# Kernel tuning notes

Hardware: AMD Instinct MI355X
Metric: run time of the kernel (lower is better)

Reference implementation:

```python
import jax, jax.numpy as jnp
import numpy as np

IN = 128; HID = 128; OUT = 128; HEADS = 3; T1 = 0.2; T2 = 0.2
B = 512; L = 32; V = 100000; NMETA = 5


def _corr_full(s, t):
    # s, t: (B, L, E, N). Full cross-correlation along last axis.
    # Matches F.conv1d(hs, ht, groups=BLE, padding=N-1): out[k] = sum_m s[k+m-(N-1)] * t[m]
    N = s.shape[-1]
    sp = jnp.pad(s, ((0, 0), (0, 0), (0, 0), (N - 1, N - 1)))
    out = jnp.stack([(sp[..., k:k + N] * t).sum(-1) for k in range(2 * N - 1)], axis=-1)
    return jnp.swapaxes(out, -1, -2)  # (B, L, 2N-1, E)


def _node_att(h, Wt, Ws, Wc):
    # h: (B, L, P, E); Wt/Ws/Wc: (HEADS, E, HID)
    Bh, Lh, P, E = h.shape
    H = h.reshape(Bh * Lh, P, E)
    hi = jnp.einsum('ne,heo->hno', H[:, 0], Wt)                 # target-node projection
    logits = jnp.einsum('npe,heo,hno->hnp', H, Ws, hi) / T1     # (heads, BL, P)
    alpha = jax.nn.softmax(logits, axis=-1)                     # softmax over path positions
    Z = jnp.einsum('hnp,npe,heo->no', alpha, H, Wc) / HEADS     # mean over heads
    return Z.reshape(Bh, Lh, -1)


def _forward(emb_user, emb_item, emb_attr1, emb_attr2, emb_attr3, Wt, Ws, Wc,
             pw1, pb1, pw2, fw1, fb1, fw2, fb2,
             UI, IU, UIUI, IUIU, UIAI1, IAIU1, UIAI2, IAIU2, UIAI3, IAIU3):
    src = emb_user[UI[:, 0, 0]]
    tgt = emb_item[IU[:, 0, 0]]
    ui = jnp.stack([emb_user[UI[..., 0]], emb_item[UI[..., 1]]], axis=3)
    iu = jnp.stack([emb_item[IU[..., 0]], emb_user[IU[..., 1]]], axis=3)

    def p4(tabs, idx):
        return jnp.stack([tabs[k][idx[..., k]] for k in range(4)], axis=3)

    uiui = p4([emb_user, emb_item, emb_user, emb_item], UIUI)
    iuiu = p4([emb_item, emb_user, emb_item, emb_user], IUIU)
    uiai1 = p4([emb_user, emb_item, emb_attr1, emb_item], UIAI1)
    iaiu1 = p4([emb_item, emb_attr1, emb_item, emb_user], IAIU1)
    uiai2 = p4([emb_user, emb_item, emb_attr2, emb_item], UIAI2)
    iaiu2 = p4([emb_item, emb_attr2, emb_item, emb_user], IAIU2)
    uiai3 = p4([emb_user, emb_item, emb_attr3, emb_item], UIAI3)
    iaiu3 = p4([emb_item, emb_attr3, emb_item, emb_user], IAIU3)

    user_feats = [ui, uiui, uiai1, uiai2, uiai3]
    item_feats = [iu, iuiu, iaiu1, iaiu2, iaiu3]
    Hs = [_node_att(_corr_full(uf, itf), Wt[m], Ws[m], Wc[m])
          for m, (uf, itf) in enumerate(zip(user_feats, item_feats))]
    Z = jnp.stack(Hs, 1)                        # (B, 5, L, HID)
    z = Z.reshape(Z.shape[0], -1, HID)          # (B, 5L, HID)
    w = jnp.tanh(z @ pw1 + pb1) @ pw2 / T2      # (B, 5L, 1)
    beta = jax.nn.softmax(w, axis=1)
    path_out = (beta * z).sum(1)                # (B, HID)
    x = jnp.concatenate([src, tgt, path_out], axis=1)
    x = jax.nn.relu(x @ fw1 + fb1)              # dropout in eval mode -> identity
    return jax.nn.sigmoid(x @ fw2 + fb2)        # (B, 1)


def setup_inputs() -> dict:
    key = jax.random.key(0)
    ks = jax.random.split(key, 24)

    def idx(k, n):
        return jax.random.randint(k, (B, L, n), 0, V, dtype=jnp.int32)

    d = {
        'UI': idx(ks[0], 2), 'IU': idx(ks[1], 2),
        'UIUI': idx(ks[2], 4), 'IUIU': idx(ks[3], 4),
        'UIAI1': idx(ks[4], 4), 'IAIU1': idx(ks[5], 4),
        'UIAI2': idx(ks[6], 4), 'IAIU2': idx(ks[7], 4),
        'UIAI3': idx(ks[8], 4), 'IAIU3': idx(ks[9], 4),
    }

    def emb(k):
        t = jax.random.normal(k, (V + 1, IN), jnp.float32) * 0.05
        return t.at[0].set(0.0)  # padding_idx=0

    d['emb_user'] = emb(ks[10]); d['emb_item'] = emb(ks[11])
    d['emb_attr1'] = emb(ks[12]); d['emb_attr2'] = emb(ks[13]); d['emb_attr3'] = emb(ks[14])
    s = (2.0 / (IN + HID)) ** 0.5  # xavier scale
    d['Wt'] = jax.random.normal(ks[15], (NMETA, HEADS, IN, HID), jnp.float32) * s
    d['Ws'] = jax.random.normal(ks[16], (NMETA, HEADS, IN, HID), jnp.float32) * s
    d['Wc'] = jax.random.normal(ks[17], (NMETA, HEADS, IN, HID), jnp.float32) * s
    d['pw1'] = jax.random.normal(ks[18], (HID, HID), jnp.float32) * s
    d['pb1'] = jnp.zeros((HID,), jnp.float32)
    d['pw2'] = jax.random.normal(ks[19], (HID, 1), jnp.float32) * s
    d['fw1'] = jax.random.normal(ks[20], (3 * HID, OUT), jnp.float32) * 0.02
    d['fb1'] = jnp.zeros((OUT,), jnp.float32)
    d['fw2'] = jax.random.normal(ks[21], (OUT, 1), jnp.float32) * 0.02
    d['fb2'] = jnp.zeros((1,), jnp.float32)
    return d


def reference(UI, IU, UIUI, IUIU, UIAI1, IAIU1, UIAI2, IAIU2, UIAI3, IAIU3,
              emb_user, emb_item, emb_attr1, emb_attr2, emb_attr3,
              Wt, Ws, Wc, pw1, pb1, pw2, fw1, fb1, fw2, fb2):
    return _forward(emb_user, emb_item, emb_attr1, emb_attr2, emb_attr3, Wt, Ws, Wc,
                    pw1, pb1, pw2, fw1, fb1, fw2, fb2,
                    UI, IU, UIUI, IUIU, UIAI1, IAIU1, UIAI2, IAIU2, UIAI3, IAIU3)
```

## Files before the change

### kernel.cpp

```cpp
#include <hip/hip_runtime.h>
#include <hip/hip_bf16.h>
#include <cstdint>
#include <cstddef>


typedef __hip_bfloat16 bf16;
typedef __attribute__((ext_vector_type(8))) short  bfrag;
typedef __attribute__((ext_vector_type(4))) float  ffrag;

#define NNODES 16384

__device__ __forceinline__ float bflo(uint32_t u) { return __uint_as_float(u << 16); }
__device__ __forceinline__ float bfhi(uint32_t u) { return __uint_as_float(u & 0xffff0000u); }

__global__ __launch_bounds__(256) void build_BmatT(
    const float* __restrict__ Ws, const float* __restrict__ Wt,
    bf16* __restrict__ BmT)
{
  int mh = blockIdx.x >> 4;
  int g  = blockIdx.x & 15;
  int m = mh / 3, h = mh % 3;
  const float* ws = Ws + (size_t)mh * 16384;
  const float* wt = Wt + (size_t)mh * 16384;
  int tid = threadIdx.x;
  int e = tid & 127, half = tid >> 7;
  __shared__ float wtl[2][128];
  for (int ep0 = g * 8; ep0 < g * 8 + 8; ep0 += 2) {
    int ep = ep0 + half;
    wtl[half][e] = wt[ep * 128 + e];
    __syncthreads();
    float acc = 0.f;
    #pragma unroll 4
    for (int o = 0; o < 128; ++o) acc += ws[e * 128 + o] * wtl[half][o];
    BmT[((size_t)(m * 384 + h * 128 + e)) * 128 + ep] = __float2bfloat16(acc);
    __syncthreads();
  }
}

__global__ __launch_bounds__(256) void conv_WcT(
    const float* __restrict__ Wc, bf16* __restrict__ WcT)
{
  int idx = blockIdx.x * 256 + threadIdx.x;
  int he = idx % 384, mo = idx / 384;
  int m = mo >> 7, o = mo & 127;
  WcT[idx] = __float2bfloat16(Wc[((size_t)m * 384 + he) * 128 + o]);
}

__global__ __launch_bounds__(256) void conv_pw1T(
    const float* __restrict__ pw1, bf16* __restrict__ pw1T)
{
  int idx = blockIdx.x * 256 + threadIdx.x;
  int o = idx >> 7, k = idx & 127;
  pw1T[idx] = __float2bfloat16(pw1[(size_t)k * 128 + o]);
}

template <int P>
__global__ __launch_bounds__(512) void fused_metapath(
    const float* __restrict__ Tu0, const float* __restrict__ Tu1,
    const float* __restrict__ Tu2, const float* __restrict__ Tu3,
    const float* __restrict__ Tt0, const float* __restrict__ Tt1,
    const float* __restrict__ Tt2, const float* __restrict__ Tt3,
    const int* __restrict__ idxU, const int* __restrict__ idxT,
    const bf16* __restrict__ BmT,
    const bf16* __restrict__ WcT,
    float* __restrict__ Zall, int m)
{
  constexpr int PP = 2 * P - 1;
  constexpr int NS = PP * 136;
  constexpr int NPAIR = 3 * PP;
  __shared__ bf16 Hs[16 * NS];
  __shared__ bf16 Ss[16 * 392];
  __shared__ float lg[16][3][8];
  __shared__ float alpha[16][3][8];

  int tid = threadIdx.x;
  int lane = tid & 63, wid = tid >> 6;
  int l15 = lane & 15, l4 = lane >> 4;
  int n0 = blockIdx.x * 16;

  {
    const float* TU[4] = {Tu0, Tu1, Tu2, Tu3};
    const float* TT[4] = {Tt0, Tt1, Tt2, Tt3};
    int e = tid & 127;
    #pragma unroll
    for (int g = 0; g < 4; ++g) {
      int ln = g * 4 + (tid >> 7);
      int n = n0 + ln;
      float su[P], st[P];
      #pragma unroll
      for (int p = 0; p < P; ++p) {
        su[p] = TU[p][(size_t)idxU[n * P + p] * 128 + e];
        st[p] = TT[p][(size_t)idxT[n * P + p] * 128 + e];
      }
      bf16* Hn = &Hs[ln * NS + e];
      #pragma unroll
      for (int k = 0; k < PP; ++k) {
        float acc = 0.f;
        #pragma unroll
        for (int i = 0; i < P; ++i) {
          int j = k + i - (P - 1);
          if (j >= 0 && j < P) acc += su[j] * st[i];
        }
        Hn[k * 136] = __float2bfloat16(acc);
      }
    }
  }
  __syncthreads();

  {
    bfrag a[4];
    #pragma unroll
    for (int kk = 0; kk < 4; ++kk)
      a[kk] = *(const bfrag*)&Hs[l15 * NS + kk * 32 + 8 * l4];
    #pragma unroll
    for (int f = 0; f < 3; ++f) {
      int col = wid * 48 + f * 16 + l15;
      ffrag acc = {0.f, 0.f, 0.f, 0.f};
      #pragma unroll
      for (int kk = 0; kk < 4; ++kk) {
        bfrag b = *(const bfrag*)&BmT[(size_t)col * 128 + kk * 32 + 8 * l4];
        acc = __builtin_amdgcn_mfma_f32_16x16x32_bf16(a[kk], b, acc, 0, 0, 0);
      }
      #pragma unroll
      for (int r = 0; r < 4; ++r) {
        int node = 4 * l4 + r;
        Ss[node * 392 + col] = __float2bfloat16(acc[r]);
      }
    }
  }
  __syncthreads();

  {
    int node = tid >> 5, q = tid & 31;
    if (q < NPAIR) {
      int h = q / PP, p = q - h * PP;
      const uint32_t* hrow = (const uint32_t*)&Hs[node * NS + p * 136];
      const uint32_t* srow = (const uint32_t*)&Ss[node * 392 + h * 128];
      float acc = 0.f;
      #pragma unroll 8
      for (int i = 0; i < 64; ++i) {
        uint32_t hv = hrow[i], sv = srow[i];
        acc += bflo(hv) * bflo(sv) + bfhi(hv) * bfhi(sv);
      }
      lg[node][h][p] = acc * 5.0f;
    }
  }
  __syncthreads();

  if (tid < 48) {
    int nd = tid / 3, h = tid - nd * 3;
    float mx = -1e30f;
    #pragma unroll
    for (int p = 0; p < PP; ++p) mx = fmaxf(mx, lg[nd][h][p]);
    float s = 0.f, ev[8];
    #pragma unroll
    for (int p = 0; p < PP; ++p) { ev[p] = expf(lg[nd][h][p] - mx); s += ev[p]; }
    float inv = 1.0f / s;
    #pragma unroll
    for (int p = 0; p < PP; ++p) alpha[nd][h][p] = ev[p] * inv;
  }
  __syncthreads();

  {
    int node = tid >> 5, q = tid & 31;
    #pragma unroll
    for (int c = 0; c < 6; ++c) {
      int o2 = q * 6 + c;
      int h = o2 >> 6, e = (o2 & 63) * 2;
      float a0 = 0.f, a1 = 0.f;
      #pragma unroll
      for (int p = 0; p < PP; ++p) {
        float al = alpha[node][h][p];
        uint32_t hv = *(const uint32_t*)&Hs[node * NS + p * 136 + e];
        a0 += al * bflo(hv);
        a1 += al * bfhi(hv);
      }
      Ss[node * 392 + h * 128 + e]     = __float2bfloat16(a0);
      Ss[node * 392 + h * 128 + e + 1] = __float2bfloat16(a1);
    }
  }
  __syncthreads();

  {
    bfrag a[12];
    #pragma unroll
    for (int kk = 0; kk < 12; ++kk)
      a[kk] = *(const bfrag*)&Ss[l15 * 392 + kk * 32 + 8 * l4];
    int col = wid * 16 + l15;
    ffrag acc = {0.f, 0.f, 0.f, 0.f};
    #pragma unroll
    for (int kk = 0; kk < 12; ++kk) {
      bfrag b = *(const bfrag*)&WcT[(size_t)col * 384 + kk * 32 + 8 * l4];
      acc = __builtin_amdgcn_mfma_f32_16x16x32_bf16(a[kk], b, acc, 0, 0, 0);
    }
    #pragma unroll
    for (int r = 0; r < 4; ++r) {
      int gn = n0 + 4 * l4 + r;
      int crow = (((gn >> 5) * 5 + m) << 5) + (gn & 31);
      Zall[(size_t)crow * 128 + col] = acc[r] * (1.0f / 3.0f);
    }
  }
}

__global__ __launch_bounds__(256) void fused_tail(
    const float* __restrict__ Zall,
    const bf16* __restrict__ pw1T,
    const float* __restrict__ pb1, const float* __restrict__ pw2,
    const int* __restrict__ UI, const int* __restrict__ IU,
    const float* __restrict__ emb_user, const float* __restrict__ emb_item,
    const float* __restrict__ fw1, const float* __restrict__ fb1,
    const float* __restrict__ fw2, const float* __restrict__ fb2,
    float* __restrict__ out)
{
  __shared__ bf16 Zs[160 * 136];
  __shared__ float wrow[160];
  __shared__ float ph[2][128];
  __shared__ float xs[384];
  __shared__ float mx_s, denom_s;
  __shared__ float yred[2];

  int b = blockIdx.x, tid = threadIdx.x;
  int lane = tid & 63, wid = tid >> 6;
  int l15 = lane & 15, l4 = lane >> 4;

  {
    const float4* src = (const float4*)(Zall + (size_t)b * 160 * 128);
    #pragma unroll
    for (int i = 0; i < 20; ++i) {
      int v = i * 256 + tid;
      int row = v >> 5, c4 = v & 31;
      float4 x = src[v];
      bf16* d = &Zs[row * 136 + c4 * 4];
      d[0] = __float2bfloat16(x.x); d[1] = __float2bfloat16(x.y);
      d[2] = __float2bfloat16(x.z); d[3] = __float2bfloat16(x.w);
    }
  }
  __syncthreads();

  for (int rf = wid; rf < 10; rf += 4) {
    bfrag a[4];
    #pragma unroll
    for (int kk = 0; kk < 4; ++kk)
      a[kk] = *(const bfrag*)&Zs[(rf * 16 + l15) * 136 + kk * 32 + 8 * l4];
    float part[4] = {0.f, 0.f, 0.f, 0.f};
    #pragma unroll
    for (int f = 0; f < 8; ++f) {
      int col = f * 16 + l15;
      ffrag acc = {0.f, 0.f, 0.f, 0.f};
      #pragma unroll
      for (int kk = 0; kk < 4; ++kk) {
        bfrag bv = *(const bfrag*)&pw1T[(size_t)col * 128 + kk * 32 + 8 * l4];
        acc = __builtin_amdgcn_mfma_f32_16x16x32_bf16(a[kk], bv, acc, 0, 0, 0);
      }
      float bias = pb1[col], w2 = pw2[col];
      #pragma unroll
      for (int r = 0; r < 4; ++r) part[r] += tanhf(acc[r] + bias) * w2;
    }
    #pragma unroll
    for (int d = 1; d < 16; d <<= 1) {
      #pragma unroll
      for (int r = 0; r < 4; ++r) part[r] += __shfl_xor(part[r], d);
    }
    if (l15 == 0) {
      #pragma unroll
      for (int r = 0; r < 4; ++r)
        wrow[rf * 16 + 4 * l4 + r] = part[r] * 5.0f;
    }
  }
  __syncthreads();

  if (tid == 0) {
    float mx = -1e30f;
    for (int j = 0; j < 160; ++j) mx = fmaxf(mx, wrow[j]);
    float s = 0.f;
    for (int j = 0; j < 160; ++j) s += expf(wrow[j] - mx);
    mx_s = mx; denom_s = s;
  }
  __syncthreads();
  {
    float mx = mx_s, inv = 1.0f / denom_s;
    if (tid < 160) wrow[tid] = expf(wrow[tid] - mx) * inv;
  }
  __syncthreads();

  {
    int e = tid & 127, half = tid >> 7;
    float acc = 0.f;
    #pragma unroll 4
    for (int j = half * 80; j < half * 80 + 80; ++j)
      acc += wrow[j] * __bfloat162float(Zs[j * 136 + e]);
    ph[half][e] = acc;
  }
  __syncthreads();

  {
    int su = UI[b * 64];
    int ti = IU[b * 64];
    if (tid < 128) {
      xs[tid]       = emb_user[(size_t)su * 128 + tid];
      xs[256 + tid] = ph[0][tid] + ph[1][tid];
    } else {
      xs[tid]       = emb_item[(size_t)ti * 128 + (tid - 128)];
    }
  }
  __syncthreads();

  {
    int o = tid & 127, half = tid >> 7;
    float acc = 0.f;
    #pragma unroll 4
    for (int i = half * 192; i < half * 192 + 192; ++i)
      acc += xs[i] * fw1[(size_t)i * 128 + o];
    __syncthreads();
    ph[half][o] = acc;
  }
  __syncthreads();
  if (tid < 128) {
    float y = fmaxf(ph[0][tid] + ph[1][tid] + fb1[tid], 0.0f) * fw2[tid];
    #pragma unroll
    for (int off = 32; off; off >>= 1) y += __shfl_down(y, off);
    if ((tid & 63) == 0) yred[tid >> 6] = y;
  }
  __syncthreads();
  if (tid == 0) {
    float s = yred[0] + yred[1] + fb2[0];
    out[b] = 1.0f / (1.0f + expf(-s));
  }
}

extern "C" void kernel_launch(void* const* d_in, const int* in_sizes, int n_in,
                              void* d_out, int out_size, void* d_ws, size_t ws_size,
                              hipStream_t stream)
{
  const int* UI    = (const int*)d_in[0];
  const int* IU    = (const int*)d_in[1];
  const int* UIUI  = (const int*)d_in[2];
  const int* IUIU  = (const int*)d_in[3];
  const int* UIAI1 = (const int*)d_in[4];
  const int* IAIU1 = (const int*)d_in[5];
  const int* UIAI2 = (const int*)d_in[6];
  const int* IAIU2 = (const int*)d_in[7];
  const int* UIAI3 = (const int*)d_in[8];
  const int* IAIU3 = (const int*)d_in[9];
  const float* emb_user = (const float*)d_in[10];
  const float* emb_item = (const float*)d_in[11];
  const float* emb_a1   = (const float*)d_in[12];
  const float* emb_a2   = (const float*)d_in[13];
  const float* emb_a3   = (const float*)d_in[14];
  const float* Wt  = (const float*)d_in[15];
  const float* Ws  = (const float*)d_in[16];
  const float* Wc  = (const float*)d_in[17];
  const float* pw1 = (const float*)d_in[18];
  const float* pb1 = (const float*)d_in[19];
  const float* pw2 = (const float*)d_in[20];
  const float* fw1 = (const float*)d_in[21];
  const float* fb1 = (const float*)d_in[22];
  const float* fw2 = (const float*)d_in[23];
  const float* fb2 = (const float*)d_in[24];
  float* out = (float*)d_out;

  char* wsb = (char*)d_ws;
  bf16*  BmT  = (bf16*)wsb;
  bf16*  WcT  = (bf16*)(wsb + 491520);
  bf16*  pw1T = (bf16*)(wsb + 983040);
  float* Zall = (float*)(wsb + 1015808);

  build_BmatT<<<240, 256, 0, stream>>>(Ws, Wt, BmT);
  conv_WcT<<<960, 256, 0, stream>>>(Wc, WcT);
  conv_pw1T<<<64, 256, 0, stream>>>(pw1, pw1T);

  const float* u2[5] = {nullptr, emb_user, emb_a1, emb_a2, emb_a3};
  const float* t1[5] = {emb_user, emb_user, emb_a1, emb_a2, emb_a3};
  const int* idxU[5] = {UI, UIUI, UIAI1, UIAI2, UIAI3};
  const int* idxT[5] = {IU, IUIU, IAIU1, IAIU2, IAIU3};

  for (int m = 0; m < 5; ++m) {
    if (m == 0) {
      fused_metapath<2><<<1024, 512, 0, stream>>>(
          emb_user, emb_item, nullptr, nullptr,
          emb_item, emb_user, nullptr, nullptr,
          idxU[m], idxT[m], BmT, WcT, Zall, m);
    } else {
      fused_metapath<4><<<1024, 512, 0, stream>>>(
          emb_user, emb_item, u2[m], emb_item,
          emb_item, t1[m], emb_item, emb_user,
          idxU[m], idxT[m],
          BmT + (size_t)m * 384 * 128, WcT + (size_t)m * 128 * 384, Zall, m);
    }
  }

  fused_tail<<<512, 256, 0, stream>>>(Zall, pw1T, pb1, pw2,
                                      UI, IU, emb_user, emb_item,
                                      fw1, fb1, fw2, fb2, out);
}
```

Measured before the change: 245.5 us.

## Merge metapath launches into one kernel, store Zall as bf16, widen tail

Replaces the five per-metapath launches with a single 5120-block kernel that picks the metapath from the block index and uses dynamic shared memory. It also hoists all embedding gathers ahead of the correlation compute so more loads are in flight, and stores the intermediate Z in bf16 to halve its traffic. The tail kernel moves to 512 threads, uses vectorized bf16 copies, and replaces the single-thread softmax with a wave-shuffle reduction. Costs are higher register pressure from the hoisted gathers, lower occupancy from the dynamic shared allocation, and bf16 rounding of Z before the tail.

```diff
diff --git a/kernel.cpp b/kernel.cpp
--- a/kernel.cpp
+++ b/kernel.cpp
@@ -55,7 +55,8 @@
 }
 
 template <int P>
-__global__ __launch_bounds__(512) void fused_metapath(
+__device__ __forceinline__ void metapath_body(
+    char* smem,
     const float* __restrict__ Tu0, const float* __restrict__ Tu1,
     const float* __restrict__ Tu2, const float* __restrict__ Tu3,
     const float* __restrict__ Tt0, const float* __restrict__ Tt1,
@@ -63,35 +64,38 @@
     const int* __restrict__ idxU, const int* __restrict__ idxT,
     const bf16* __restrict__ BmT,
     const bf16* __restrict__ WcT,
-    float* __restrict__ Zall, int m)
+    bf16* __restrict__ Zall, int m, int tile)
 {
   constexpr int PP = 2 * P - 1;
   constexpr int NS = PP * 136;
   constexpr int NPAIR = 3 * PP;
-  __shared__ bf16 Hs[16 * NS];
-  __shared__ bf16 Ss[16 * 392];
-  __shared__ float lg[16][3][8];
-  __shared__ float alpha[16][3][8];
+  bf16*  Hs    = (bf16*)smem;
+  bf16*  Ss    = (bf16*)(smem + 16 * NS * 2);
+  float* lg    = (float*)(smem + 16 * NS * 2 + 16 * 392 * 2);
+  float* alpha = lg + 16 * 3 * 8;
 
   int tid = threadIdx.x;
   int lane = tid & 63, wid = tid >> 6;
   int l15 = lane & 15, l4 = lane >> 4;
-  int n0 = blockIdx.x * 16;
+  int n0 = tile * 16;
 
   {
     const float* TU[4] = {Tu0, Tu1, Tu2, Tu3};
     const float* TT[4] = {Tt0, Tt1, Tt2, Tt3};
     int e = tid & 127;
+    float su[4][P], st[4][P];
+    #pragma unroll
+    for (int g = 0; g < 4; ++g) {
+      int n = n0 + g * 4 + (tid >> 7);
+      #pragma unroll
+      for (int p = 0; p < P; ++p) {
+        su[g][p] = TU[p][(size_t)idxU[n * P + p] * 128 + e];
+        st[g][p] = TT[p][(size_t)idxT[n * P + p] * 128 + e];
+      }
+    }
     #pragma unroll
     for (int g = 0; g < 4; ++g) {
       int ln = g * 4 + (tid >> 7);
-      int n = n0 + ln;
-      float su[P], st[P];
-      #pragma unroll
-      for (int p = 0; p < P; ++p) {
-        su[p] = TU[p][(size_t)idxU[n * P + p] * 128 + e];
-        st[p] = TT[p][(size_t)idxT[n * P + p] * 128 + e];
-      }
       bf16* Hn = &Hs[ln * NS + e];
       #pragma unroll
       for (int k = 0; k < PP; ++k) {
@@ -99,7 +103,7 @@
         #pragma unroll
         for (int i = 0; i < P; ++i) {
           int j = k + i - (P - 1);
-          if (j >= 0 && j < P) acc += su[j] * st[i];
+          if (j >= 0 && j < P) acc += su[g][j] * st[g][i];
         }
         Hn[k * 136] = __float2bfloat16(acc);
       }
@@ -142,22 +146,21 @@
         uint32_t hv = hrow[i], sv = srow[i];
         acc += bflo(hv) * bflo(sv) + bfhi(hv) * bfhi(sv);
       }
-      lg[node][h][p] = acc * 5.0f;
+      lg[(node * 3 + h) * 8 + p] = acc * 5.0f;
     }
   }
   __syncthreads();
 
   if (tid < 48) {
-    int nd = tid / 3, h = tid - nd * 3;
     float mx = -1e30f;
     #pragma unroll
-    for (int p = 0; p < PP; ++p) mx = fmaxf(mx, lg[nd][h][p]);
+    for (int p = 0; p < PP; ++p) mx = fmaxf(mx, lg[tid * 8 + p]);
     float s = 0.f, ev[8];
     #pragma unroll
-    for (int p = 0; p < PP; ++p) { ev[p] = expf(lg[nd][h][p] - mx); s += ev[p]; }
+    for (int p = 0; p < PP; ++p) { ev[p] = expf(lg[tid * 8 + p] - mx); s += ev[p]; }
     float inv = 1.0f / s;
     #pragma unroll
-    for (int p = 0; p < PP; ++p) alpha[nd][h][p] = ev[p] * inv;
+    for (int p = 0; p < PP; ++p) alpha[tid * 8 + p] = ev[p] * inv;
   }
   __syncthreads();
 
@@ -170,7 +173,7 @@
       float a0 = 0.f, a1 = 0.f;
       #pragma unroll
       for (int p = 0; p < PP; ++p) {
-        float al = alpha[node][h][p];
+        float al = alpha[(node * 3 + h) * 8 + p];
         uint32_t hv = *(const uint32_t*)&Hs[node * NS + p * 136 + e];
         a0 += al * bflo(hv);
         a1 += al * bfhi(hv);
@@ -197,13 +200,47 @@
     for (int r = 0; r < 4; ++r) {
       int gn = n0 + 4 * l4 + r;
       int crow = (((gn >> 5) * 5 + m) << 5) + (gn & 31);
-      Zall[(size_t)crow * 128 + col] = acc[r] * (1.0f / 3.0f);
-    }
-  }
-}
-
-__global__ __launch_bounds__(256) void fused_tail(
-    const float* __restrict__ Zall,
+      Zall[(size_t)crow * 128 + col] = __float2bfloat16(acc[r] * (1.0f / 3.0f));
+    }
+  }
+}
+
+__global__ __launch_bounds__(512) void fused_all(
+    const float* __restrict__ emb_user, const float* __restrict__ emb_item,
+    const float* __restrict__ emb_a1, const float* __restrict__ emb_a2,
+    const float* __restrict__ emb_a3,
+    const int* __restrict__ UI,    const int* __restrict__ IU,
+    const int* __restrict__ UIUI,  const int* __restrict__ IUIU,
+    const int* __restrict__ UIAI1, const int* __restrict__ IAIU1,
+    const int* __restrict__ UIAI2, const int* __restrict__ IAIU2,
+    const int* __restrict__ UIAI3, const int* __restrict__ IAIU3,
+    const bf16* __restrict__ BmT, const bf16* __restrict__ WcT,
+    bf16* __restrict__ Zall)
+{
+  extern __shared__ char smem[];
+  int bid = blockIdx.x;
+  int m = bid >> 10, tile = bid & 1023;
+  if (m == 0) {
+    metapath_body<2>(smem, emb_user, emb_item, nullptr, nullptr,
+                     emb_item, emb_user, nullptr, nullptr,
+                     UI, IU, BmT, WcT, Zall, 0, tile);
+  } else {
+    const float* u2 = (m == 1) ? emb_user : (m == 2) ? emb_a1
+                    : (m == 3) ? emb_a2 : emb_a3;
+    const int* iu_ = (m == 1) ? UIUI : (m == 2) ? UIAI1
+                   : (m == 3) ? UIAI2 : UIAI3;
+    const int* it_ = (m == 1) ? IUIU : (m == 2) ? IAIU1
+                   : (m == 3) ? IAIU2 : IAIU3;
+    metapath_body<4>(smem, emb_user, emb_item, u2, emb_item,
+                     emb_item, u2, emb_item, emb_user,
+                     iu_, it_,
+                     BmT + (size_t)m * 49152, WcT + (size_t)m * 49152,
+                     Zall, m, tile);
+  }
+}
+
+__global__ __launch_bounds__(512) void fused_tail(
+    const bf16* __restrict__ Zall,
     const bf16* __restrict__ pw1T,
     const float* __restrict__ pb1, const float* __restrict__ pw2,
     const int* __restrict__ UI, const int* __restrict__ IU,
@@ -214,9 +251,9 @@
 {
   __shared__ bf16 Zs[160 * 136];
   __shared__ float wrow[160];
-  __shared__ float ph[2][128];
+  __shared__ float ph[4][128];
   __shared__ float xs[384];
-  __shared__ float mx_s, denom_s;
+  __shared__ float sred[16];
   __shared__ float yred[2];
 
   int b = blockIdx.x, tid = threadIdx.x;
@@ -225,19 +262,19 @@
 
   {
     const float4* src = (const float4*)(Zall + (size_t)b * 160 * 128);
-    #pragma unroll
-    for (int i = 0; i < 20; ++i) {
-      int v = i * 256 + tid;
-      int row = v >> 5, c4 = v & 31;
-      float4 x = src[v];
-      bf16* d = &Zs[row * 136 + c4 * 4];
-      d[0] = __float2bfloat16(x.x); d[1] = __float2bfloat16(x.y);
-      d[2] = __float2bfloat16(x.z); d[3] = __float2bfloat16(x.w);
-    }
-  }
-  __syncthreads();
-
-  for (int rf = wid; rf < 10; rf += 4) {
+    float4 v[5];
+    #pragma unroll
+    for (int i = 0; i < 5; ++i) v[i] = src[i * 512 + tid];
+    #pragma unroll
+    for (int i = 0; i < 5; ++i) {
+      int idx = i * 512 + tid;
+      int row = idx >> 4, c8 = idx & 15;
+      *(float4*)&Zs[row * 136 + c8 * 8] = v[i];
+    }
+  }
+  __syncthreads();
+
+  for (int rf = wid; rf < 10; rf += 8) {
     bfrag a[4];
     #pragma unroll
     for (int kk = 0; kk < 4; ++kk)
@@ -269,27 +306,44 @@
   }
   __syncthreads();
 
-  if (tid == 0) {
-    float mx = -1e30f;
-    for (int j = 0; j < 160; ++j) mx = fmaxf(mx, wrow[j]);
-    float s = 0.f;
-    for (int j = 0; j < 160; ++j) s += expf(wrow[j] - mx);
-    mx_s = mx; denom_s = s;
-  }
-  __syncthreads();
-  {
-    float mx = mx_s, inv = 1.0f / denom_s;
-    if (tid < 160) wrow[tid] = expf(wrow[tid] - mx) * inv;
-  }
-  __syncthreads();
-
-  {
-    int e = tid & 127, half = tid >> 7;
+  {
+    float v = (tid < 160) ? wrow[tid] : -1e30f;
+    #pragma unroll
+    for (int off = 32; off; off >>= 1) v = fmaxf(v, __shfl_xor(v, off));
+    if (lane == 0) sred[wid] = v;
+    __syncthreads();
+    if (tid < 64) {
+      float mval = (lane < 8) ? sred[lane] : -1e30f;
+      #pragma unroll
+      for (int off = 4; off; off >>= 1) mval = fmaxf(mval, __shfl_xor(mval, off));
+      if (lane == 0) sred[8] = mval;
+    }
+    __syncthreads();
+    float mx = sred[8];
+    float ev = (tid < 160) ? expf(wrow[tid] - mx) : 0.f;
+    float s = ev;
+    #pragma unroll
+    for (int off = 32; off; off >>= 1) s += __shfl_xor(s, off);
+    if (lane == 0) sred[wid] = s;
+    __syncthreads();
+    if (tid < 64) {
+      float sval = (lane < 8) ? sred[lane] : 0.f;
+      #pragma unroll
+      for (int off = 4; off; off >>= 1) sval += __shfl_xor(sval, off);
+      if (lane == 0) sred[9] = sval;
+    }
+    __syncthreads();
+    if (tid < 160) wrow[tid] = ev / sred[9];
+  }
+  __syncthreads();
+
+  {
+    int e = tid & 127, q = tid >> 7;
     float acc = 0.f;
     #pragma unroll 4
-    for (int j = half * 80; j < half * 80 + 80; ++j)
+    for (int j = q * 40; j < q * 40 + 40; ++j)
       acc += wrow[j] * __bfloat162float(Zs[j * 136 + e]);
-    ph[half][e] = acc;
+    ph[q][e] = acc;
   }
   __syncthreads();
 
@@ -297,26 +351,28 @@
     int su = UI[b * 64];
     int ti = IU[b * 64];
     if (tid < 128) {
-      xs[tid]       = emb_user[(size_t)su * 128 + tid];
-      xs[256 + tid] = ph[0][tid] + ph[1][tid];
-    } else {
-      xs[tid]       = emb_item[(size_t)ti * 128 + (tid - 128)];
-    }
-  }
-  __syncthreads();
-
-  {
-    int o = tid & 127, half = tid >> 7;
+      xs[256 + tid] = ph[0][tid] + ph[1][tid] + ph[2][tid] + ph[3][tid];
+    } else if (tid < 256) {
+      xs[tid - 128] = emb_user[(size_t)su * 128 + (tid - 128)];
+    } else if (tid < 384) {
+      xs[tid - 128] = emb_item[(size_t)ti * 128 + (tid - 256)];
+    }
+  }
+  __syncthreads();
+
+  {
+    int o = tid & 127, q = tid >> 7;
     float acc = 0.f;
     #pragma unroll 4
-    for (int i = half * 192; i < half * 192 + 192; ++i)
+    for (int i = q * 96; i < q * 96 + 96; ++i)
       acc += xs[i] * fw1[(size_t)i * 128 + o];
     __syncthreads();
-    ph[half][o] = acc;
+    ph[q][o] = acc;
   }
   __syncthreads();
   if (tid < 128) {
-    float y = fmaxf(ph[0][tid] + ph[1][tid] + fb1[tid], 0.0f) * fw2[tid];
+    float y = fmaxf(ph[0][tid] + ph[1][tid] + ph[2][tid] + ph[3][tid] + fb1[tid],
+                    0.0f) * fw2[tid];
     #pragma unroll
     for (int off = 32; off; off >>= 1) y += __shfl_down(y, off);
     if ((tid & 63) == 0) yred[tid >> 6] = y;
@@ -363,33 +419,18 @@
   bf16*  BmT  = (bf16*)wsb;
   bf16*  WcT  = (bf16*)(wsb + 491520);
   bf16*  pw1T = (bf16*)(wsb + 983040);
-  float* Zall = (float*)(wsb + 1015808);
+  bf16*  Zall = (bf16*)(wsb + 1015808);
 
   build_BmatT<<<240, 256, 0, stream>>>(Ws, Wt, BmT);
   conv_WcT<<<960, 256, 0, stream>>>(Wc, WcT);
   conv_pw1T<<<64, 256, 0, stream>>>(pw1, pw1T);
 
-  const float* u2[5] = {nullptr, emb_user, emb_a1, emb_a2, emb_a3};
-  const float* t1[5] = {emb_user, emb_user, emb_a1, emb_a2, emb_a3};
-  const int* idxU[5] = {UI, UIUI, UIAI1, UIAI2, UIAI3};
-  const int* idxT[5] = {IU, IUIU, IAIU1, IAIU2, IAIU3};
-
-  for (int m = 0; m < 5; ++m) {
-    if (m == 0) {
-      fused_metapath<2><<<1024, 512, 0, stream>>>(
-          emb_user, emb_item, nullptr, nullptr,
-          emb_item, emb_user, nullptr, nullptr,
-          idxU[m], idxT[m], BmT, WcT, Zall, m);
-    } else {
-      fused_metapath<4><<<1024, 512, 0, stream>>>(
-          emb_user, emb_item, u2[m], emb_item,
-          emb_item, t1[m], emb_item, emb_user,
-          idxU[m], idxT[m],
-          BmT + (size_t)m * 384 * 128, WcT + (size_t)m * 128 * 384, Zall, m);
-    }
-  }
-
-  fused_tail<<<512, 256, 0, stream>>>(Zall, pw1T, pb1, pw2,
+  fused_all<<<5120, 512, 46080, stream>>>(
+      emb_user, emb_item, emb_a1, emb_a2, emb_a3,
+      UI, IU, UIUI, IUIU, UIAI1, IAIU1, UIAI2, IAIU2, UIAI3, IAIU3,
+      BmT, WcT, Zall);
+
+  fused_tail<<<512, 512, 0, stream>>>(Zall, pw1T, pb1, pw2,
                                       UI, IU, emb_user, emb_item,
                                       fw1, fb1, fw2, fb2, out);
 }
```

Measured after the change: 216.3 us. 11.9% less time.
